# Performance work log

Measured on AMD Instinct MI355X. Metric: run time of the kernel, lower is better.

The kernel has to match this reference:

```python
import jax, jax.numpy as jnp
import numpy as np

EPS = 1e-5

def _conv3x3(x, w):
    # x: [B,C,H,W], w: [O,I,3,3], stride 1, padding 1
    return jax.lax.conv_general_dilated(
        x, w, window_strides=(1, 1), padding=((1, 1), (1, 1)),
        dimension_numbers=('NCHW', 'OIHW', 'NCHW'))

def _bn(x, gamma, beta, mean, var):
    inv = gamma / jnp.sqrt(var + EPS)
    return x * inv[None, :, None, None] + (beta - mean * inv)[None, :, None, None]

def setup_inputs() -> dict:
    key = jax.random.key(0)
    ks = jax.random.split(key, 6)
    B, C, H, W, E = 32, 64, 112, 112, 10
    x = jax.random.normal(ks[0], (B, C, H, W), dtype=jnp.float32)
    w1 = jax.random.normal(ks[1], (E, C, C, 3, 3), dtype=jnp.float32) * 0.05
    w2 = jax.random.normal(ks[2], (E, C, C, 3, 3), dtype=jnp.float32) * 0.05
    alpha = jax.random.uniform(ks[3], (E,), dtype=jnp.float32)
    return {
        'x': x, 'w1': w1, 'w2': w2, 'alpha': alpha,
        'bn1_gamma': jnp.ones((C,), jnp.float32),
        'bn1_beta': jnp.zeros((C,), jnp.float32),
        'bn1_mean': jnp.zeros((C,), jnp.float32),
        'bn1_var': jax.random.uniform(ks[4], (C,), jnp.float32) + 0.5,
        'bn2_gamma': jnp.ones((C,), jnp.float32),
        'bn2_beta': jnp.zeros((C,), jnp.float32),
        'bn2_mean': jnp.zeros((C,), jnp.float32),
        'bn2_var': jax.random.uniform(ks[5], (C,), jnp.float32) + 0.5,
    }

def reference(x, w1, w2, alpha,
              bn1_gamma, bn1_beta, bn1_mean, bn1_var,
              bn2_gamma, bn2_beta, bn2_mean, bn2_var):
    # Convolution is linear in its weights, so sum_i alpha[i] * conv(x, w_i)
    # == conv(x, sum_i alpha[i] * w_i): pre-combine experts into one kernel.
    w1_eff = jnp.einsum('e,eoihw->oihw', alpha, w1)
    w2_eff = jnp.einsum('e,eoihw->oihw', alpha, w2)
    out = _conv3x3(x, w1_eff)
    out = jax.nn.relu(_bn(out, bn1_gamma, bn1_beta, bn1_mean, bn1_var))
    out = _conv3x3(out, w2_eff)
    out = _bn(out, bn2_gamma, bn2_beta, bn2_mean, bn2_var)
    return jax.nn.relu(out + x)
```

## Files before the change

### kernel.cpp

```cpp
#include <hip/hip_runtime.h>


typedef __bf16 bf16x8 __attribute__((ext_vector_type(8)));
typedef float f32x4 __attribute__((ext_vector_type(4)));
typedef unsigned short u16;
typedef u16 u16x8 __attribute__((ext_vector_type(8)));

#define NH 112
#define NW 112
#define PH 114
#define PW 114
#define PROWB (PW * 128)
#define BUFB 23040

__device__ __forceinline__ u16 f2b(float f) {
  unsigned u = __builtin_bit_cast(unsigned, f);
  u += 0x7FFFu + ((u >> 16) & 1u);
  return (u16)(u >> 16);
}
__device__ __forceinline__ float b2f(u16 b) {
  unsigned u = ((unsigned)b) << 16;
  return __builtin_bit_cast(float, u);
}

__device__ __forceinline__ void gl_lds16(const void* g, void* l) {
  __builtin_amdgcn_global_load_lds(
      (const __attribute__((address_space(1))) unsigned int*)g,
      (__attribute__((address_space(3))) unsigned int*)l, 16, 0, 0);
}

__global__ void border_zero(u16* __restrict__ a, u16* __restrict__ bbuf) {
  int idx = blockIdx.x * 256 + threadIdx.x;
  if (idx >= 231424) return;
  int c8 = idx & 7;
  int t = idx >> 3;
  int buf = t >= 14464;
  t -= buf * 14464;
  int img = t / 452, e = t % 452;
  int h, w;
  if (e < 114) { h = 0; w = e; }
  else if (e < 228) { h = 113; w = e - 114; }
  else if (e < 340) { h = e - 227; w = 0; }
  else { h = e - 339; w = 113; }
  u16* base = buf ? bbuf : a;
  u16x8 z = {0, 0, 0, 0, 0, 0, 0, 0};
  *reinterpret_cast<u16x8*>(base + (((long)img * PH + h) * PW + w) * 64 + c8 * 8) = z;
}

__global__ __launch_bounds__(256) void transform_kernel(const float* __restrict__ x,
                                                        u16* __restrict__ xpad) {
  __shared__ alignas(16) u16 t[7168];
  int tid = threadIdx.x, bid = blockIdx.x;
  int b = bid / NH, h = bid % NH;
  const float* src = x + (long)b * 64 * 12544 + h * NW;
  f32x4 v[7];
#pragma unroll
  for (int it = 0; it < 7; ++it) {
    int fid = it * 256 + tid;
    int c = fid / 28, wq = fid % 28;
    v[it] = *reinterpret_cast<const f32x4*>(src + c * 12544 + wq * 4);
  }
#pragma unroll
  for (int it = 0; it < 7; ++it) {
    int fid = it * 256 + tid;
    int c = fid / 28, wq = fid % 28;
    int key = (wq & 7) << 4;
#pragma unroll
    for (int j = 0; j < 4; ++j) {
      int px = wq * 4 + j;
      *reinterpret_cast<u16*>((char*)t + px * 128 + ((c * 2) ^ key)) = f2b(v[it][j]);
    }
  }
  __syncthreads();
  int hp = h + 1;
  u16* rowb = xpad + (((long)b * PH + hp) * PW) * 64;
#pragma unroll
  for (int it = 0; it < 4; ++it) {
    int cidx = it * 256 + tid;
    if (cidx < 896) {
      int c8 = cidx & 7, px = cidx >> 3;
      int lchunk = c8 ^ ((px >> 2) & 7);
      u16x8 vv = *reinterpret_cast<const u16x8*>((const char*)t + px * 128 + lchunk * 16);
      int wp = px + 1;
      int gkey = (2 * hp + wp) & 7;
      *reinterpret_cast<u16x8*>(rowb + (long)wp * 64 + ((c8 ^ gkey) * 8)) = vv;
    }
  }
}

__global__ void prep_kernel(
    const float* __restrict__ w1, const float* __restrict__ w2,
    const float* __restrict__ alpha,
    const float* __restrict__ g1, const float* __restrict__ b1,
    const float* __restrict__ m1, const float* __restrict__ v1,
    const float* __restrict__ g2, const float* __restrict__ b2,
    const float* __restrict__ m2, const float* __restrict__ v2,
    u16* __restrict__ weff1, u16* __restrict__ weff2, float* __restrict__ bnc) {
  int idx = blockIdx.x * 256 + threadIdx.x;
  if (idx < 36864) {
    int i = idx & 63;
    int o = (idx >> 6) & 63;
    int kpos = idx >> 12;
    int base = (o * 64 + i) * 9 + kpos;
    float a1 = 0.f, a2 = 0.f;
#pragma unroll
    for (int e = 0; e < 10; ++e) {
      float al = alpha[e];
      a1 += al * w1[e * 36864 + base];
      a2 += al * w2[e * 36864 + base];
    }
    weff1[idx] = f2b(a1);
    weff2[idx] = f2b(a2);
  }
  if (blockIdx.x == 0 && threadIdx.x < 64) {
    int c = threadIdx.x;
    float i1 = g1[c] * rsqrtf(v1[c] + 1e-5f);
    float i2 = g2[c] * rsqrtf(v2[c] + 1e-5f);
    bnc[c] = i1;
    bnc[64 + c] = b1[c] - m1[c] * i1;
    bnc[128 + c] = i2;
    bnc[192 + c] = b2[c] - m2[c] * i2;
  }
}

template <int PASS, int RESID>
__global__ __launch_bounds__(256, 2) void conv_bn_kernel(
    const u16* __restrict__ xin, const float* __restrict__ x,
    const u16* __restrict__ xres, const u16* __restrict__ weff,
    const float* __restrict__ bnc, u16* __restrict__ ypad,
    float* __restrict__ out) {
  __shared__ alignas(64) char smem[2 * BUFB];

  int tid = threadIdx.x, lane = tid & 63, wv = tid >> 6;
  int ol = lane & 15, kg = (lane >> 4) & 3;
  const int o = wv * 16 + ol;

  float inv = bnc[PASS * 128 + o];
  float bias = bnc[PASS * 128 + 64 + o];

  bf16x8 wf[3][3][2];
#pragma unroll
  for (int kh = 0; kh < 3; ++kh)
#pragma unroll
    for (int kw = 0; kw < 3; ++kw)
#pragma unroll
      for (int ks = 0; ks < 2; ++ks)
        wf[kh][kw][ks] = __builtin_bit_cast(
            bf16x8, *reinterpret_cast<const u16x8*>(
                        weff + (((kh * 3 + kw) * 64 + o) * 64 + ks * 32 + kg * 8)));
  asm volatile("s_waitcnt vmcnt(0)" ::: "memory");
  __builtin_amdgcn_sched_barrier(0);

  int sb = (blockIdx.x & 7) * 196 + (blockIdx.x >> 3);
  int tb[2], th0[2], tw0[2];
#pragma unroll
  for (int t = 0; t < 2; ++t) {
    int tt = sb * 2 + t;
    tb[t] = tt / 98;
    int r = tt % 98;
    th0[t] = (r / 7) * 8;
    tw0[t] = (r % 7) * 16;
  }

  auto stage = [&](int t, int boff) {
#pragma unroll
    for (int k = 0; k < 6; ++k) {
      int i = wv + k * 4;
      if (i < 23) {
        int cb = i * 64 + lane;
        if (cb < 1440) {
          int row = cb / 144, rem = cb % 144;
          gl_lds16((const char*)(xin + (((long)tb[t] * PH + th0[t]) * PW + tw0[t]) * 64) +
                       (long)row * PROWB + rem * 16,
                   smem + boff + cb * 16);
        }
      }
    }
  };

  stage(0, 0);
  asm volatile("" ::: "memory");
  stage(1, BUFB);
  asm volatile("" ::: "memory");
  if (wv < 3) asm volatile("s_waitcnt vmcnt(6)" ::: "memory");
  else        asm volatile("s_waitcnt vmcnt(5)" ::: "memory");
  __builtin_amdgcn_sched_barrier(0);

#pragma unroll
  for (int t = 0; t < 2; ++t) {
    const int boff = t * BUFB;
    __builtin_amdgcn_s_barrier();
    __builtin_amdgcn_sched_barrier(0);

    f32x4 acc[8];
#pragma unroll
    for (int mf = 0; mf < 8; ++mf) acc[mf] = f32x4{0.f, 0.f, 0.f, 0.f};

#pragma unroll
    for (int kw = 0; kw < 3; ++kw)
#pragma unroll
      for (int ks = 0; ks < 2; ++ks) {
        const int col = ol + kw;
        const int sb8 = (ks << 2) | kg;
        bf16x8 a[4];
#pragma unroll
        for (int u = 0; u < 3; ++u) {
          int slot = sb8 ^ ((2 * u + col) & 7);
          a[u] = *reinterpret_cast<const bf16x8*>(smem + boff + (u * 18 + col) * 128 +
                                                  slot * 16);
        }
#pragma unroll
        for (int mf = 0; mf < 8; ++mf) {
          if (mf < 7) {
            int rr = mf + 3;
            int slot = sb8 ^ ((2 * rr + col) & 7);
            a[(mf + 3) & 3] = *reinterpret_cast<const bf16x8*>(
                smem + boff + (rr * 18 + col) * 128 + slot * 16);
          }
          acc[mf] = __builtin_amdgcn_mfma_f32_16x16x32_bf16(a[mf & 3], wf[0][kw][ks],
                                                            acc[mf], 0, 0, 0);
          acc[mf] = __builtin_amdgcn_mfma_f32_16x16x32_bf16(a[(mf + 1) & 3], wf[1][kw][ks],
                                                            acc[mf], 0, 0, 0);
          acc[mf] = __builtin_amdgcn_mfma_f32_16x16x32_bf16(a[(mf + 2) & 3], wf[2][kw][ks],
                                                            acc[mf], 0, 0, 0);
        }
      }

    if (t == 0) {
      asm volatile("s_waitcnt vmcnt(0)" ::: "memory");
      __builtin_amdgcn_sched_barrier(0);
    }

    if constexpr (PASS == 0) {
      __builtin_amdgcn_sched_barrier(0);
      __builtin_amdgcn_s_barrier();
      __builtin_amdgcn_sched_barrier(0);
      u16* ys = reinterpret_cast<u16*>(smem + boff);
#pragma unroll
      for (int mf = 0; mf < 8; ++mf)
#pragma unroll
        for (int rg = 0; rg < 4; ++rg) {
          int p = mf * 16 + kg * 4 + rg;
          ys[p * 72 + o] = f2b(fmaxf(acc[mf][rg] * inv + bias, 0.f));
        }
      asm volatile("s_waitcnt lgkmcnt(0)" ::: "memory");
      __builtin_amdgcn_sched_barrier(0);
      __builtin_amdgcn_s_barrier();
      __builtin_amdgcn_sched_barrier(0);
#pragma unroll
      for (int it = 0; it < 4; ++it) {
        int cidx = it * 256 + tid;
        int c8 = cidx & 7, p = cidx >> 3;
        int hp = th0[t] + (p >> 4) + 1, wp = tw0[t] + (p & 15) + 1;
        int gkey = (2 * hp + wp) & 7;
        *reinterpret_cast<u16x8*>(ypad + (((long)tb[t] * PH + hp) * PW + wp) * 64 +
                                  ((c8 ^ gkey) * 8)) =
            *reinterpret_cast<const u16x8*>(ys + p * 72 + c8 * 8);
      }
    } else {
#pragma unroll
      for (int half = 0; half < 2; ++half) {
        f32x4 xr[4];
        if constexpr (RESID == 0) {
#pragma unroll
          for (int m = 0; m < 4; ++m) {
            int h = th0[t] + half * 4 + m;
            xr[m] = *reinterpret_cast<const f32x4*>(
                x + (((tb[t] * 64 + o) * NH + h) * NW + tw0[t] + kg * 4));
          }
        } else {
#pragma unroll
          for (int m = 0; m < 4; ++m) {
            int hp = th0[t] + half * 4 + m + 1;
#pragma unroll
            for (int rg = 0; rg < 4; ++rg) {
              int wp = tw0[t] + kg * 4 + rg + 1;
              int key = (2 * hp + wp) & 7;
              u16 bv = xres[(((long)tb[t] * PH + hp) * PW + wp) * 64 +
                            ((o >> 3) ^ key) * 8 + (o & 7)];
              xr[m][rg] = b2f(bv);
            }
          }
        }
#pragma unroll
        for (int m = 0; m < 4; ++m) {
          int mf = half * 4 + m;
          int h = th0[t] + mf;
          f32x4 vv;
#pragma unroll
          for (int rg = 0; rg < 4; ++rg)
            vv[rg] = fmaxf(acc[mf][rg] * inv + bias + xr[m][rg], 0.f);
          *reinterpret_cast<f32x4*>(
              out + (((tb[t] * 64 + o) * NH + h) * NW + tw0[t] + kg * 4)) = vv;
        }
      }
    }
  }
}

extern "C" void kernel_launch(void* const* d_in, const int* in_sizes, int n_in,
                              void* d_out, int out_size, void* d_ws, size_t ws_size,
                              hipStream_t stream) {
  const float* x = (const float*)d_in[0];
  const float* w1 = (const float*)d_in[1];
  const float* w2 = (const float*)d_in[2];
  const float* alpha = (const float*)d_in[3];
  const float* g1 = (const float*)d_in[4];
  const float* b1 = (const float*)d_in[5];
  const float* m1 = (const float*)d_in[6];
  const float* v1 = (const float*)d_in[7];
  const float* g2 = (const float*)d_in[8];
  const float* b2 = (const float*)d_in[9];
  const float* m2 = (const float*)d_in[10];
  const float* v2 = (const float*)d_in[11];
  float* out = (float*)d_out;

  char* ws = (char*)d_ws;
  u16* weff1 = (u16*)ws;
  u16* weff2 = (u16*)(ws + 73728);
  float* bnc = (float*)(ws + 147456);
  u16* y1pad = (u16*)(ws + 148480);
  const size_t PADB = 53231616ull;
  bool big = ws_size >= 148480ull + 2ull * PADB;
  u16* xpad = big ? (u16*)(ws + 148480 + PADB) : (u16*)d_out;

  border_zero<<<904, 256, 0, stream>>>(xpad, y1pad);
  transform_kernel<<<32 * NH, 256, 0, stream>>>(x, xpad);
  prep_kernel<<<144, 256, 0, stream>>>(w1, w2, alpha, g1, b1, m1, v1,
                                       g2, b2, m2, v2, weff1, weff2, bnc);
  conv_bn_kernel<0, 0><<<1568, 256, 0, stream>>>(xpad, x, nullptr, weff1, bnc,
                                                 y1pad, nullptr);
  if (big)
    conv_bn_kernel<1, 1><<<1568, 256, 0, stream>>>(y1pad, x, xpad, weff2, bnc,
                                                   nullptr, out);
  else
    conv_bn_kernel<1, 0><<<1568, 256, 0, stream>>>(y1pad, x, nullptr, weff2, bnc,
                                                   nullptr, out);
}
```

Measured before the change: 134.3 us.

## Split conv kernels; pipeline four tiles per block and stage residual via LDS

```diff
diff --git a/kernel.cpp b/kernel.cpp
--- a/kernel.cpp
+++ b/kernel.cpp
@@ -12,6 +12,9 @@
 #define PW 114
 #define PROWB (PW * 128)
 #define BUFB 23040
+
+#define WAITVM(n) asm volatile("s_waitcnt vmcnt(" #n ")" ::: "memory")
+#define SCHEDB __builtin_amdgcn_sched_barrier(0)
 
 __device__ __forceinline__ u16 f2b(float f) {
   unsigned u = __builtin_bit_cast(unsigned, f);
@@ -123,20 +126,17 @@
   }
 }
 
-template <int PASS, int RESID>
-__global__ __launch_bounds__(256, 2) void conv_bn_kernel(
-    const u16* __restrict__ xin, const float* __restrict__ x,
-    const u16* __restrict__ xres, const u16* __restrict__ weff,
-    const float* __restrict__ bnc, u16* __restrict__ ypad,
-    float* __restrict__ out) {
+__global__ __launch_bounds__(256, 2) void conv_p0_kernel(
+    const u16* __restrict__ xin, const u16* __restrict__ weff,
+    const float* __restrict__ bnc, u16* __restrict__ ypad) {
   __shared__ alignas(64) char smem[2 * BUFB];
 
   int tid = threadIdx.x, lane = tid & 63, wv = tid >> 6;
   int ol = lane & 15, kg = (lane >> 4) & 3;
   const int o = wv * 16 + ol;
 
-  float inv = bnc[PASS * 128 + o];
-  float bias = bnc[PASS * 128 + 64 + o];
+  float inv = bnc[o];
+  float bias = bnc[64 + o];
 
   bf16x8 wf[3][3][2];
 #pragma unroll
@@ -149,7 +149,7 @@
             bf16x8, *reinterpret_cast<const u16x8*>(
                         weff + (((kh * 3 + kw) * 64 + o) * 64 + ks * 32 + kg * 8)));
   asm volatile("s_waitcnt vmcnt(0)" ::: "memory");
-  __builtin_amdgcn_sched_barrier(0);
+  SCHEDB;
 
   int sb = (blockIdx.x & 7) * 196 + (blockIdx.x >> 3);
   int tb[2], th0[2], tw0[2];
@@ -182,15 +182,15 @@
   asm volatile("" ::: "memory");
   stage(1, BUFB);
   asm volatile("" ::: "memory");
-  if (wv < 3) asm volatile("s_waitcnt vmcnt(6)" ::: "memory");
-  else        asm volatile("s_waitcnt vmcnt(5)" ::: "memory");
-  __builtin_amdgcn_sched_barrier(0);
+  if (wv < 3) WAITVM(6);
+  else        WAITVM(5);
+  SCHEDB;
 
 #pragma unroll
   for (int t = 0; t < 2; ++t) {
     const int boff = t * BUFB;
     __builtin_amdgcn_s_barrier();
-    __builtin_amdgcn_sched_barrier(0);
+    SCHEDB;
 
     f32x4 acc[8];
 #pragma unroll
@@ -228,59 +228,184 @@
 
     if (t == 0) {
       asm volatile("s_waitcnt vmcnt(0)" ::: "memory");
-      __builtin_amdgcn_sched_barrier(0);
-    }
-
-    if constexpr (PASS == 0) {
-      __builtin_amdgcn_sched_barrier(0);
-      __builtin_amdgcn_s_barrier();
-      __builtin_amdgcn_sched_barrier(0);
-      u16* ys = reinterpret_cast<u16*>(smem + boff);
-#pragma unroll
-      for (int mf = 0; mf < 8; ++mf)
+      SCHEDB;
+    }
+
+    SCHEDB;
+    __builtin_amdgcn_s_barrier();
+    SCHEDB;
+    u16* ys = reinterpret_cast<u16*>(smem + boff);
+#pragma unroll
+    for (int mf = 0; mf < 8; ++mf)
+#pragma unroll
+      for (int rg = 0; rg < 4; ++rg) {
+        int p = mf * 16 + kg * 4 + rg;
+        ys[p * 72 + o] = f2b(fmaxf(acc[mf][rg] * inv + bias, 0.f));
+      }
+    asm volatile("s_waitcnt lgkmcnt(0)" ::: "memory");
+    SCHEDB;
+    __builtin_amdgcn_s_barrier();
+    SCHEDB;
+#pragma unroll
+    for (int it = 0; it < 4; ++it) {
+      int cidx = it * 256 + tid;
+      int c8 = cidx & 7, p = cidx >> 3;
+      int hp = th0[t] + (p >> 4) + 1, wp = tw0[t] + (p & 15) + 1;
+      int gkey = (2 * hp + wp) & 7;
+      *reinterpret_cast<u16x8*>(ypad + (((long)tb[t] * PH + hp) * PW + wp) * 64 +
+                                ((c8 ^ gkey) * 8)) =
+          *reinterpret_cast<const u16x8*>(ys + p * 72 + c8 * 8);
+    }
+  }
+}
+
+template <int RESID>
+__global__ __launch_bounds__(256, 2) void conv_p1_kernel(
+    const u16* __restrict__ yin, const float* __restrict__ x,
+    const u16* __restrict__ xres, const u16* __restrict__ weff,
+    const float* __restrict__ bnc, float* __restrict__ out) {
+  constexpr int BUF = RESID ? (BUFB + 16384) : BUFB;
+  __shared__ alignas(64) char smem[2 * BUF];
+
+  int tid = threadIdx.x, lane = tid & 63, wv = tid >> 6;
+  int ol = lane & 15, kg = (lane >> 4) & 3;
+  const int o = wv * 16 + ol;
+
+  float inv = bnc[128 + o];
+  float bias = bnc[192 + o];
+
+  bf16x8 wf[3][3][2];
+#pragma unroll
+  for (int kh = 0; kh < 3; ++kh)
+#pragma unroll
+    for (int kw = 0; kw < 3; ++kw)
+#pragma unroll
+      for (int ks = 0; ks < 2; ++ks)
+        wf[kh][kw][ks] = __builtin_bit_cast(
+            bf16x8, *reinterpret_cast<const u16x8*>(
+                        weff + (((kh * 3 + kw) * 64 + o) * 64 + ks * 32 + kg * 8)));
+  asm volatile("s_waitcnt vmcnt(0)" ::: "memory");
+  SCHEDB;
+
+  int sb = (blockIdx.x & 7) * 98 + (blockIdx.x >> 3);
+  int tb[4], th0[4], tw0[4];
+#pragma unroll
+  for (int t = 0; t < 4; ++t) {
+    int tt = sb * 4 + t;
+    tb[t] = tt / 98;
+    int r = tt % 98;
+    th0[t] = (r / 7) * 8;
+    tw0[t] = (r % 7) * 16;
+  }
+
+  auto stage = [&](int t, int boff) {
+#pragma unroll
+    for (int k = 0; k < 6; ++k) {
+      int i = wv + k * 4;
+      if (i < 23) {
+        int cb = i * 64 + lane;
+        if (cb < 1440) {
+          int row = cb / 144, rem = cb % 144;
+          gl_lds16((const char*)(yin + (((long)tb[t] * PH + th0[t]) * PW + tw0[t]) * 64) +
+                       (long)row * PROWB + rem * 16,
+                   smem + boff + cb * 16);
+        }
+      }
+    }
+    if constexpr (RESID) {
+#pragma unroll
+      for (int k = 0; k < 4; ++k) {
+        int i = wv + k * 4;
+        int cr = i * 64 + lane;
+        int rp = cr >> 7, rem = cr & 127;
+        gl_lds16((const char*)xres +
+                     (((long)tb[t] * PH + th0[t] + 1 + rp) * PW + tw0[t] + 1) * 128 +
+                     rem * 16,
+                 smem + boff + BUFB + cr * 16);
+      }
+    }
+  };
+  auto gateS = [&] {
+    if constexpr (RESID) {
+      if (wv < 3) WAITVM(10); else WAITVM(9);
+    } else {
+      if (wv < 3) WAITVM(6); else WAITVM(5);
+    }
+  };
+
+  stage(0, 0);
+  asm volatile("" ::: "memory");
+  stage(1, BUF);
+  asm volatile("" ::: "memory");
+  gateS();
+  SCHEDB;
+
+#pragma unroll
+  for (int t = 0; t < 4; ++t) {
+    const int boff = (t & 1) * BUF;
+    __builtin_amdgcn_s_barrier();
+    SCHEDB;
+
+    f32x4 acc[8];
+#pragma unroll
+    for (int mf = 0; mf < 8; ++mf) acc[mf] = f32x4{0.f, 0.f, 0.f, 0.f};
+
+#pragma unroll
+    for (int kw = 0; kw < 3; ++kw)
+#pragma unroll
+      for (int ks = 0; ks < 2; ++ks) {
+        const int col = ol + kw;
+        const int sb8 = (ks << 2) | kg;
+        bf16x8 a[4];
+#pragma unroll
+        for (int u = 0; u < 3; ++u) {
+          int slot = sb8 ^ ((2 * u + col) & 7);
+          a[u] = *reinterpret_cast<const bf16x8*>(smem + boff + (u * 18 + col) * 128 +
+                                                  slot * 16);
+        }
+#pragma unroll
+        for (int mf = 0; mf < 8; ++mf) {
+          if (mf < 7) {
+            int rr = mf + 3;
+            int slot = sb8 ^ ((2 * rr + col) & 7);
+            a[(mf + 3) & 3] = *reinterpret_cast<const bf16x8*>(
+                smem + boff + (rr * 18 + col) * 128 + slot * 16);
+          }
+          acc[mf] = __builtin_amdgcn_mfma_f32_16x16x32_bf16(a[mf & 3], wf[0][kw][ks],
+                                                            acc[mf], 0, 0, 0);
+          acc[mf] = __builtin_amdgcn_mfma_f32_16x16x32_bf16(a[(mf + 1) & 3], wf[1][kw][ks],
+                                                            acc[mf], 0, 0, 0);
+          acc[mf] = __builtin_amdgcn_mfma_f32_16x16x32_bf16(a[(mf + 2) & 3], wf[2][kw][ks],
+                                                            acc[mf], 0, 0, 0);
+        }
+      }
+
+    if constexpr (RESID) {
+#pragma unroll
+      for (int mf = 0; mf < 8; ++mf) {
+        int h = th0[t] + mf, hp = h + 1;
+        f32x4 vv;
 #pragma unroll
         for (int rg = 0; rg < 4; ++rg) {
-          int p = mf * 16 + kg * 4 + rg;
-          ys[p * 72 + o] = f2b(fmaxf(acc[mf][rg] * inv + bias, 0.f));
-        }
-      asm volatile("s_waitcnt lgkmcnt(0)" ::: "memory");
-      __builtin_amdgcn_sched_barrier(0);
-      __builtin_amdgcn_s_barrier();
-      __builtin_amdgcn_sched_barrier(0);
-#pragma unroll
-      for (int it = 0; it < 4; ++it) {
-        int cidx = it * 256 + tid;
-        int c8 = cidx & 7, p = cidx >> 3;
-        int hp = th0[t] + (p >> 4) + 1, wp = tw0[t] + (p & 15) + 1;
-        int gkey = (2 * hp + wp) & 7;
-        *reinterpret_cast<u16x8*>(ypad + (((long)tb[t] * PH + hp) * PW + wp) * 64 +
-                                  ((c8 ^ gkey) * 8)) =
-            *reinterpret_cast<const u16x8*>(ys + p * 72 + c8 * 8);
+          int wq = kg * 4 + rg, wp = tw0[t] + wq + 1;
+          int key = (2 * hp + wp) & 7;
+          u16 bv = *reinterpret_cast<const u16*>(
+              smem + boff + BUFB + (mf * 16 + wq) * 128 + (((o >> 3) ^ key) * 16) +
+              (o & 7) * 2);
+          vv[rg] = fmaxf(acc[mf][rg] * inv + bias + b2f(bv), 0.f);
+        }
+        *reinterpret_cast<f32x4*>(out + (((tb[t] * 64 + o) * NH + h) * NW + tw0[t] +
+                                         kg * 4)) = vv;
       }
     } else {
 #pragma unroll
       for (int half = 0; half < 2; ++half) {
         f32x4 xr[4];
-        if constexpr (RESID == 0) {
-#pragma unroll
-          for (int m = 0; m < 4; ++m) {
-            int h = th0[t] + half * 4 + m;
-            xr[m] = *reinterpret_cast<const f32x4*>(
-                x + (((tb[t] * 64 + o) * NH + h) * NW + tw0[t] + kg * 4));
-          }
-        } else {
-#pragma unroll
-          for (int m = 0; m < 4; ++m) {
-            int hp = th0[t] + half * 4 + m + 1;
-#pragma unroll
-            for (int rg = 0; rg < 4; ++rg) {
-              int wp = tw0[t] + kg * 4 + rg + 1;
-              int key = (2 * hp + wp) & 7;
-              u16 bv = xres[(((long)tb[t] * PH + hp) * PW + wp) * 64 +
-                            ((o >> 3) ^ key) * 8 + (o & 7)];
-              xr[m][rg] = b2f(bv);
-            }
-          }
+#pragma unroll
+        for (int m = 0; m < 4; ++m) {
+          int h = th0[t] + half * 4 + m;
+          xr[m] = *reinterpret_cast<const f32x4*>(
+              x + (((tb[t] * 64 + o) * NH + h) * NW + tw0[t] + kg * 4));
         }
 #pragma unroll
         for (int m = 0; m < 4; ++m) {
@@ -295,6 +420,17 @@
         }
       }
     }
+
+    SCHEDB;
+    __builtin_amdgcn_s_barrier();
+    SCHEDB;
+    if (t + 2 < 4) stage(t + 2, boff);
+    if (t < 2) {
+      gateS();
+    } else if (t == 2) {
+      WAITVM(0);
+    }
+    SCHEDB;
   }
 }
 
@@ -328,12 +464,9 @@
   transform_kernel<<<32 * NH, 256, 0, stream>>>(x, xpad);
   prep_kernel<<<144, 256, 0, stream>>>(w1, w2, alpha, g1, b1, m1, v1,
                                        g2, b2, m2, v2, weff1, weff2, bnc);
-  conv_bn_kernel<0, 0><<<1568, 256, 0, stream>>>(xpad, x, nullptr, weff1, bnc,
-                                                 y1pad, nullptr);
+  conv_p0_kernel<<<1568, 256, 0, stream>>>(xpad, weff1, bnc, y1pad);
   if (big)
-    conv_bn_kernel<1, 1><<<1568, 256, 0, stream>>>(y1pad, x, xpad, weff2, bnc,
-                                                   nullptr, out);
+    conv_p1_kernel<1><<<784, 256, 0, stream>>>(y1pad, x, xpad, weff2, bnc, out);
   else
-    conv_bn_kernel<1, 0><<<1568, 256, 0, stream>>>(y1pad, x, nullptr, weff2, bnc,
-                                                   nullptr, out);
-}
+    conv_p1_kernel<0><<<784, 256, 0, stream>>>(y1pad, x, nullptr, weff2, bnc, out);
+}
```

After: 133.9 us. No clear change (-0.3%).
